# Kernel tuning notes

Measured on AMD Instinct MI355X. Metric: run time of the kernel, lower is better.

The kernel has to match this reference:

```python
import jax, jax.numpy as jnp
import numpy as np

SCORE_THRESH = 0.05
IOU_THRESH = 0.5
TOP_K = 1000      # candidates fed to NMS
MAX_DET = 100     # padded output detections


def _build_anchors(H, W):
    """Standard RetinaNet anchors: levels P3..P7, 3 ratios x 3 scales."""
    ratios = np.array([0.5, 1.0, 2.0])
    scales = np.array([2 ** 0, 2 ** (1.0 / 3.0), 2 ** (2.0 / 3.0)])
    all_anchors = []
    for lvl in [3, 4, 5, 6, 7]:
        stride = 2 ** lvl
        base_size = 2 ** (lvl + 2)
        # 9 base anchors centered at origin (ratio-major, scale-minor ordering)
        s = base_size * np.tile(scales, len(ratios))          # [9]
        r = np.repeat(ratios, len(scales))                    # [9]
        areas = s * s
        w = np.sqrt(areas / r)
        h = w * r
        base = np.stack([-w / 2, -h / 2, w / 2, h / 2], axis=1)  # [9,4]
        fh = (H + stride - 1) // stride
        fw = (W + stride - 1) // stride
        sx = (np.arange(fw) + 0.5) * stride
        sy = (np.arange(fh) + 0.5) * stride
        gx, gy = np.meshgrid(sx, sy)
        shifts = np.stack([gx.ravel(), gy.ravel(), gx.ravel(), gy.ravel()], axis=1)  # [fh*fw,4]
        all_anchors.append((shifts[:, None, :] + base[None, :, :]).reshape(-1, 4))
    return np.concatenate(all_anchors, axis=0).astype(np.float32)  # [A,4]


def setup_inputs() -> dict:
    key = jax.random.key(0)
    k1, k2 = jax.random.split(key)
    H = W = 1024
    C = 80
    anchors = jnp.asarray(_build_anchors(H, W))[None]            # [1,A,4]
    A = anchors.shape[1]
    classifications = jax.random.uniform(k1, (1, A, C), dtype=jnp.float32)
    regressions = jax.random.normal(k2, (1, A, 4), dtype=jnp.float32)
    return {"classifications": classifications, "regressions": regressions,
            "anchors": anchors, "img_h": H, "img_w": W}


def _decode_clip(anchors, regressions, img_h, img_w):
    # BBoxTransform with mean 0, std [0.1,0.1,0.2,0.2]
    aw = anchors[..., 2] - anchors[..., 0]
    ah = anchors[..., 3] - anchors[..., 1]
    acx = anchors[..., 0] + 0.5 * aw
    acy = anchors[..., 1] + 0.5 * ah
    dx = regressions[..., 0] * 0.1
    dy = regressions[..., 1] * 0.1
    dw = regressions[..., 2] * 0.2
    dh = regressions[..., 3] * 0.2
    pcx = acx + dx * aw
    pcy = acy + dy * ah
    pw = jnp.exp(dw) * aw
    ph = jnp.exp(dh) * ah
    boxes = jnp.stack([pcx - 0.5 * pw, pcy - 0.5 * ph,
                       pcx + 0.5 * pw, pcy + 0.5 * ph], axis=-1)
    # ClipBoxes
    lo = jnp.zeros(4, boxes.dtype)
    hi = jnp.array([img_w, img_h, img_w, img_h], boxes.dtype)
    return jnp.clip(boxes, lo, hi)  # [1,A,4]


def _nms_keep(boxes, valid):
    """Sequential greedy NMS over score-sorted boxes [K,4]; returns keep mask [K]."""
    K = boxes.shape[0]
    areas = jnp.maximum(boxes[:, 2] - boxes[:, 0], 0) * jnp.maximum(boxes[:, 3] - boxes[:, 1], 0)
    idx = jnp.arange(K)

    def body(i, keep):
        b = boxes[i]
        xx1 = jnp.maximum(b[0], boxes[:, 0])
        yy1 = jnp.maximum(b[1], boxes[:, 1])
        xx2 = jnp.minimum(b[2], boxes[:, 2])
        yy2 = jnp.minimum(b[3], boxes[:, 3])
        inter = jnp.maximum(xx2 - xx1, 0) * jnp.maximum(yy2 - yy1, 0)
        iou = inter / (areas[i] + areas - inter + 1e-8)
        suppress = (iou > IOU_THRESH) & (idx > i)
        return jnp.where(keep[i], keep & ~suppress, keep)

    return jax.lax.fori_loop(0, K, body, valid)


def reference(classifications, regressions, anchors, img_h, img_w):
    boxes = _decode_clip(anchors, regressions, img_h, img_w)       # [1,A,4]
    scores = jnp.max(classifications, axis=2)                      # [1,A]
    # Score threshold: mask out low scores, keep fixed shape (padded NMS)
    s0 = jnp.where(scores[0] > SCORE_THRESH, scores[0], -1.0)      # [A]
    top_scores, top_idx = jax.lax.top_k(s0, TOP_K)                 # sorted desc
    cand_boxes = boxes[0, top_idx]                                 # [K,4]
    keep = _nms_keep(cand_boxes, top_scores > SCORE_THRESH)        # [K]
    final = jnp.where(keep, top_scores, -1.0)
    det_scores, sel = jax.lax.top_k(final, MAX_DET)                # [100]
    det_idx = top_idx[sel]                                         # indices into A
    det_valid = det_scores > SCORE_THRESH
    cls = classifications[0, det_idx]                              # [100,C]
    nms_scores = jnp.where(det_valid, jnp.max(cls, axis=1), 0.0)
    nms_class = jnp.where(det_valid, jnp.argmax(cls, axis=1), -1)
    det_boxes = jnp.where(det_valid[:, None], boxes[0, det_idx], 0.0)
    return (nms_scores, nms_class, det_boxes)
```

## Files before the change

kernel.cpp:

```cpp
#include <hip/hip_runtime.h>
#include <stdint.h>

#define SCORE_THRESH 0.05f
#define IOU_THRESH 0.5f
#define TOP_K 1000
#define MAX_DET 100

#define D0_BITS 13
#define D0_BINS 8192
#define D1_BITS 12
#define D1_BINS 4096
#define NREP 4
#define CAND_CAP 2048
#define NMS_CHUNK 128

typedef unsigned int u32;
typedef unsigned long long u64;

#define OFF_HIST0    0
#define OFF_HIST1    131072
#define OFF_STATE    196608
#define OFF_BAR      197632
#define MEMSET_LEN   218112
#define OFF_CAND     218112
#define OFF_RFLAG    226304
#define OFF_SIDX     230304
#define OFF_SSCORE   234304
#define OFF_CBOX     238304
#define OFF_M        254304
#define OFF_SCORES   382304

#define BAR_STRIDE_U32 1024

__device__ __forceinline__ u32 order_f32(float f) {
    u32 b = __float_as_uint(f);
    return (b & 0x80000000u) ? ~b : (b | 0x80000000u);
}

__device__ __forceinline__ void st_sc(u32* p, u32 v)   { __hip_atomic_store(p, v, __ATOMIC_RELAXED, __HIP_MEMORY_SCOPE_AGENT); }
__device__ __forceinline__ void st_sc(float* p, float v){ __hip_atomic_store(p, v, __ATOMIC_RELAXED, __HIP_MEMORY_SCOPE_AGENT); }
__device__ __forceinline__ void st_sc(u64* p, u64 v)   { __hip_atomic_store(p, v, __ATOMIC_RELAXED, __HIP_MEMORY_SCOPE_AGENT); }
__device__ __forceinline__ u32  ld_sc(u32* p)          { return __hip_atomic_load(p, __ATOMIC_RELAXED, __HIP_MEMORY_SCOPE_AGENT); }

__device__ __forceinline__ void gbar(u32* barr, int k, int b, u32 gsz, bool dowait) {
    __syncthreads();
    if (threadIdx.x == 0) {
        asm volatile("s_waitcnt vmcnt(0)" ::: "memory");
        u32* base = barr + (size_t)k * BAR_STRIDE_U32;
        int g = b & 7;
        if (__hip_atomic_fetch_add(base + g * 32, 1u, __ATOMIC_RELAXED,
                                   __HIP_MEMORY_SCOPE_AGENT) == gsz - 1u)
            __hip_atomic_fetch_add(base + 8 * 32, 1u, __ATOMIC_RELAXED,
                                   __HIP_MEMORY_SCOPE_AGENT);
        if (dowait) {
            while (ld_sc(base + 8 * 32) < 8u)
                __builtin_amdgcn_s_sleep(8);
        }
        asm volatile("" ::: "memory");
    }
    __syncthreads();
}

union ShMem {
    u32 hl[D0_BINS / 2];
    u32 wtot[4];
    struct { u32 wcnt[4]; u32 wbase[4]; u32 bbase; } cmp;
    struct { u64 ckeys[8]; u32 wpart[4][8]; } rank;
    struct {
        u64 Ml[2 * NMS_CHUNK * 16];
        u64 keepS[16];
        u32 nib[256];
        int act[TOP_K];
        u32 wsum[4];
        int nactS;
        int det[MAX_DET];
    } nms;
};

__global__ void __launch_bounds__(256, 2)
mega(const float* __restrict__ cls, const float* __restrict__ regs,
     const float* __restrict__ anchors, const int* __restrict__ pH,
     const int* __restrict__ pW, int A, int C,
     char* __restrict__ ws, float* __restrict__ out)
{
    __shared__ ShMem sh;
    __shared__ u32 shcut[3];
    u32*   hist0  = (u32*)(ws + OFF_HIST0);
    u32*   hist1  = (u32*)(ws + OFF_HIST1);
    u32*   state  = (u32*)(ws + OFF_STATE);
    u32*   barr   = (u32*)(ws + OFF_BAR);
    u32*   cand   = (u32*)(ws + OFF_CAND);
    u32*   rflag  = (u32*)(ws + OFF_RFLAG);
    u32*   sidx   = (u32*)(ws + OFF_SIDX);
    float* sscore = (float*)(ws + OFF_SSCORE);
    float* cbox   = (float*)(ws + OFF_CBOX);
    u64*   M      = (u64*)(ws + OFF_M);
    float* scores = (float*)(ws + OFF_SCORES);

    const int t = threadIdx.x;
    const int b = blockIdx.x;
    const int G = gridDim.x;
    const int gid = b * 256 + t;
    const int gstride = G * 256;
    const int lane = t & 63, wv = t >> 6;
    const u32 gsz = (u32)(G >> 3);

    if (C == 80) {
        for (int i = t; i < D0_BINS / 2; i += 256) sh.hl[i] = 0;
        __syncthreads();
        int sub = t & 3;
        int la  = t >> 2;
        int nstrips = (A + 63) >> 6;
        int per = (nstrips + G - 1) / G;
        for (int s = 0; s < per; s++) {
            int a = (b * per + s) * 64 + la;
            float m = -1e30f;
            if (a < A) {
                const float* p = cls + (size_t)a * 80 + sub * 4;
                #pragma unroll
                for (int k2 = 0; k2 < 5; k2++) {
                    float4 v = *(const float4*)(p + k2 * 16);
                    m = fmaxf(m, fmaxf(fmaxf(v.x, v.y), fmaxf(v.z, v.w)));
                }
            }
            m = fmaxf(m, __shfl_xor(m, 1, 64));
            m = fmaxf(m, __shfl_xor(m, 2, 64));
            if (sub == 0 && a < A) {
                float s0 = (m > SCORE_THRESH) ? m : -1.0f;
                st_sc(&scores[a], s0);
                u32 d = order_f32(s0) >> (32 - D0_BITS);
                atomicAdd(&sh.hl[d >> 1], (d & 1) ? 0x10000u : 1u);
            }
        }
        __syncthreads();
        u32* rep = hist0 + (size_t)(b & (NREP - 1)) * D0_BINS;
        for (int i = t; i < D0_BINS / 2; i += 256) {
            u32 v = sh.hl[i];
            if (v & 0xFFFFu) atomicAdd(&rep[2 * i],     v & 0xFFFFu);
            if (v >> 16)     atomicAdd(&rep[2 * i + 1], v >> 16);
        }
    } else {
        u32* rep = hist0 + (size_t)(b & (NREP - 1)) * D0_BINS;
        for (int a = gid; a < A; a += gstride) {
            const float* p = cls + (size_t)a * C;
            float m = -1e30f;
            for (int c = 0; c < C; c++) m = fmaxf(m, p[c]);
            float s0 = (m > SCORE_THRESH) ? m : -1.0f;
            st_sc(&scores[a], s0);
            atomicAdd(&rep[order_f32(s0) >> (32 - D0_BITS)], 1u);
        }
    }
    gbar(barr, 0, b, gsz, true);

    {
        u32 cnt[32];
        #pragma unroll
        for (int i = 0; i < 32; i++) cnt[i] = 0;
        const uint4* hp = (const uint4*)hist0;
        #pragma unroll
        for (int r = 0; r < NREP; r++) {
            #pragma unroll
            for (int i = 0; i < 8; i++) {
                uint4 v = hp[r * (D0_BINS / 4) + t * 8 + i];
                cnt[4*i]   += v.x; cnt[4*i+1] += v.y;
                cnt[4*i+2] += v.z; cnt[4*i+3] += v.w;
            }
        }
        u32 s = 0;
        #pragma unroll
        for (int i = 0; i < 32; i++) s += cnt[i];
        u32 x = s;
        for (int off = 1; off < 64; off <<= 1) {
            u32 v = (u32)__shfl_down((int)x, off, 64);
            if (lane + off < 64) x += v;
        }
        if (lane == 0) sh.wtot[wv] = x;
        __syncthreads();
        u32 above = x - s;
        for (int w = wv + 1; w < 4; w++) above += sh.wtot[w];
        if (above < TOP_K && above + s >= TOP_K) {
            u32 cum = above;
            for (int i = 31; i >= 0; i--) {
                cum += cnt[i];
                if (cum >= TOP_K) {
                    shcut[0] = (u32)(t * 32 + i);
                    shcut[1] = TOP_K - (cum - cnt[i]);
                    break;
                }
            }
        }
        __syncthreads();
    }
    const u32 d0cut = shcut[0];
    const u32 krem  = shcut[1];

    {
        u32* rep1 = hist1 + (size_t)(b & (NREP - 1)) * D1_BINS;
        for (int a = gid; a < A; a += gstride) {
            u32 key = order_f32(scores[a]);
            if ((key >> (32 - D0_BITS)) == d0cut)
                atomicAdd(&rep1[(key >> 7) & (D1_BINS - 1)], 1u);
        }
    }
    gbar(barr, 1, b, gsz, true);

    {
        u32 cnt[16];
        #pragma unroll
        for (int i = 0; i < 16; i++) cnt[i] = 0;
        const uint4* hp = (const uint4*)hist1;
        #pragma unroll
        for (int r = 0; r < NREP; r++) {
            #pragma unroll
            for (int i = 0; i < 4; i++) {
                uint4 v = hp[r * (D1_BINS / 4) + t * 4 + i];
                cnt[4*i]   += v.x; cnt[4*i+1] += v.y;
                cnt[4*i+2] += v.z; cnt[4*i+3] += v.w;
            }
        }
        u32 s = 0;
        #pragma unroll
        for (int i = 0; i < 16; i++) s += cnt[i];
        u32 x = s;
        for (int off = 1; off < 64; off <<= 1) {
            u32 v = (u32)__shfl_down((int)x, off, 64);
            if (lane + off < 64) x += v;
        }
        if (lane == 0) sh.wtot[wv] = x;
        __syncthreads();
        u32 above = x - s;
        for (int w = wv + 1; w < 4; w++) above += sh.wtot[w];
        if (above < krem && above + s >= krem) {
            u32 cum = above;
            for (int i = 15; i >= 0; i--) {
                cum += cnt[i];
                if (cum >= krem) { shcut[2] = (u32)(t * 16 + i); break; }
            }
        }
        __syncthreads();
    }
    const u32 cut25 = (d0cut << D1_BITS) | shcut[2];

    {
        int nr = (A + gstride - 1) / gstride;
        u32 mycnt = 0;
        for (int r = 0; r < nr; r++) {
            int a = gid + r * gstride;
            mycnt += ((a < A) && ((order_f32(scores[a]) >> 7) >= cut25)) ? 1u : 0u;
        }
        u32 wc = mycnt;
        wc += (u32)__shfl_xor((int)wc, 1, 64);
        wc += (u32)__shfl_xor((int)wc, 2, 64);
        wc += (u32)__shfl_xor((int)wc, 4, 64);
        wc += (u32)__shfl_xor((int)wc, 8, 64);
        wc += (u32)__shfl_xor((int)wc, 16, 64);
        wc += (u32)__shfl_xor((int)wc, 32, 64);
        if (lane == 0) sh.cmp.wcnt[wv] = wc;
        __syncthreads();
        if (t == 0) {
            u32 s = 0;
            #pragma unroll
            for (int w = 0; w < 4; w++) { sh.cmp.wbase[w] = s; s += sh.cmp.wcnt[w]; }
            sh.cmp.bbase = s ? atomicAdd(&state[5 * 32], s) : 0u;
        }
        __syncthreads();
        u32 off = sh.cmp.bbase + sh.cmp.wbase[wv];
        for (int r = 0; r < nr; r++) {
            int a = gid + r * gstride;
            bool pass = (a < A) && ((order_f32(scores[a]) >> 7) >= cut25);
            u64 mask = __ballot(pass ? 1 : 0);
            if (pass) {
                u32 pos = off + (u32)__popcll(mask & ((1ull << lane) - 1ull));
                if (pos < CAND_CAP) st_sc(&cand[pos], (u32)a);
            }
            off += (u32)__popcll(mask);
        }
    }
    gbar(barr, 2, b, gsz, b < CAND_CAP / 8);

    if (b < CAND_CAP / 8) {
        int n = (int)state[5 * 32]; if (n > CAND_CAP) n = CAND_CAP;
        u64 kj[8];
        #pragma unroll
        for (int q = 0; q < 8; q++) {
            int j = t * 8 + q;
            u64 kk = 0ull;
            if (j < n) {
                u32 a = cand[j];
                kk = ((u64)order_f32(scores[a]) << 32) | (u64)(0xFFFFFFFFu - a);
            }
            kj[q] = kk;
        }
        for (int bb = b; bb < CAND_CAP / 8; bb += G) {
            if (t < 8) {
                int c = bb * 8 + t;
                u64 ck = 0ull;
                if (c < n) {
                    u32 a = cand[c];
                    ck = ((u64)order_f32(scores[a]) << 32) | (u64)(0xFFFFFFFFu - a);
                }
                sh.rank.ckeys[t] = ck;
            }
            __syncthreads();
            u64 ck[8];
            #pragma unroll
            for (int q = 0; q < 8; q++) ck[q] = sh.rank.ckeys[q];
            u32 cnt8[8] = {0,0,0,0,0,0,0,0};
            #pragma unroll
            for (int q = 0; q < 8; q++) {
                u64 kq = kj[q];
                #pragma unroll
                for (int q2 = 0; q2 < 8; q2++) cnt8[q2] += (kq > ck[q2]) ? 1u : 0u;
            }
            #pragma unroll
            for (int q2 = 0; q2 < 8; q2++) {
                u32 x = cnt8[q2];
                x += (u32)__shfl_xor((int)x, 1, 64);
                x += (u32)__shfl_xor((int)x, 2, 64);
                x += (u32)__shfl_xor((int)x, 4, 64);
                x += (u32)__shfl_xor((int)x, 8, 64);
                x += (u32)__shfl_xor((int)x, 16, 64);
                x += (u32)__shfl_xor((int)x, 32, 64);
                if (lane == 0) sh.rank.wpart[wv][q2] = x;
            }
            __syncthreads();
            if (t < 8) {
                int c = bb * 8 + t;
                if (c < n) {
                    u32 rank = sh.rank.wpart[0][t] + sh.rank.wpart[1][t]
                             + sh.rank.wpart[2][t] + sh.rank.wpart[3][t];
                    if (rank < TOP_K) {
                        u32 a = cand[c];
                        st_sc(&sidx[rank], a);
                        st_sc(&sscore[rank], scores[a]);
                        float4 an = *(const float4*)(anchors + (size_t)a * 4);
                        float4 rg = *(const float4*)(regs + (size_t)a * 4);
                        float aw = an.z - an.x, ah = an.w - an.y;
                        float acx = an.x + 0.5f * aw, acy = an.y + 0.5f * ah;
                        float pcx = acx + (rg.x * 0.1f) * aw;
                        float pcy = acy + (rg.y * 0.1f) * ah;
                        float pw = expf(rg.z * 0.2f) * aw;
                        float ph = expf(rg.w * 0.2f) * ah;
                        float W = (float)(*pW), H = (float)(*pH);
                        st_sc(&cbox[rank * 4 + 0], fminf(fmaxf(pcx - 0.5f * pw, 0.0f), W));
                        st_sc(&cbox[rank * 4 + 1], fminf(fmaxf(pcy - 0.5f * ph, 0.0f), H));
                        st_sc(&cbox[rank * 4 + 2], fminf(fmaxf(pcx + 0.5f * pw, 0.0f), W));
                        st_sc(&cbox[rank * 4 + 3], fminf(fmaxf(pcy + 0.5f * ph, 0.0f), H));
                    }
                }
            }
            __syncthreads();
        }
    }
    gbar(barr, 3, b, gsz, b * 4 < TOP_K);

    {
        const float4* B4 = (const float4*)cbox;
        for (int i = b * 4 + wv; i < TOP_K; i += G * 4) {
            float4 bi = B4[i];
            float ai = fmaxf(bi.z - bi.x, 0.0f) * fmaxf(bi.w - bi.y, 0.0f);
            u64 any = 0ull;
            for (int w = 0; w < 16; w++) {
                int j = w * 64 + lane;
                bool sup = false;
                if (j < TOP_K && j > i) {
                    float4 bj = B4[j];
                    float aj = fmaxf(bj.z - bj.x, 0.0f) * fmaxf(bj.w - bj.y, 0.0f);
                    float xx1 = fmaxf(bi.x, bj.x), yy1 = fmaxf(bi.y, bj.y);
                    float xx2 = fminf(bi.z, bj.z), yy2 = fminf(bi.w, bj.w);
                    float inter = fmaxf(xx2 - xx1, 0.0f) * fmaxf(yy2 - yy1, 0.0f);
                    float iou = inter / (ai + aj - inter + 1e-8f);
                    sup = iou > IOU_THRESH;
                }
                u64 mask = __ballot(sup ? 1 : 0);
                if (lane == 0) { st_sc(&M[(size_t)i * 16 + w], mask); any |= mask; }
            }
            if (lane == 0) st_sc(&rflag[i], (any != 0ull) ? 1u : 0u);
        }
    }
    gbar(barr, 4, b, gsz, b == 0);

    if (b == 0) {
        {
            u32 nb = 0;
            int j0 = 4 * t;
            #pragma unroll
            for (int q = 0; q < 4; q++) {
                int j = j0 + q;
                if (j < TOP_K && sscore[j] > SCORE_THRESH) nb |= (1u << q);
            }
            sh.nms.nib[t] = nb;
        }
        u32 flags = 0; int cnt = 0;
        {
            int r0 = 4 * t;
            #pragma unroll
            for (int q = 0; q < 4; q++) {
                int r = r0 + q;
                if (r < TOP_K && rflag[r]) { flags |= (1u << q); cnt++; }
            }
        }
        int x = cnt;
        for (int off = 1; off < 64; off <<= 1) {
            int v = __shfl_up(x, off, 64);
            if (lane >= off) x += v;
        }
        if (lane == 63) sh.nms.wsum[wv] = (u32)x;
        __syncthreads();
        if (t < 16) {
            u64 w = 0;
            for (int m2 = 0; m2 < 16; m2++)
                w |= ((u64)sh.nms.nib[t * 16 + m2]) << (4 * m2);
            sh.nms.keepS[t] = w;
        }
        int base = 0;
        for (int w = 0; w < wv; w++) base += (int)sh.nms.wsum[w];
        int pos = base + x - cnt;
        {
            int r0 = 4 * t;
            #pragma unroll
            for (int q = 0; q < 4; q++)
                if (flags & (1u << q)) sh.nms.act[pos++] = r0 + q;
        }
        if (t == 0) {
            int na = 0;
            for (int w = 0; w < 4; w++) na += (int)sh.nms.wsum[w];
            sh.nms.nactS = na;
        }
        __syncthreads();
        int nact = sh.nms.nactS;
        int nchunks = (nact + NMS_CHUNK - 1) / NMS_CHUNK;

        if (nchunks > 0) {
            int cn0 = (nact < NMS_CHUNK) ? nact : NMS_CHUNK;
            for (int i = t; i < cn0 * 16; i += 256) {
                int row = sh.nms.act[i >> 4];
                sh.nms.Ml[i] = M[(size_t)row * 16 + (i & 15)];
            }
        }
        __syncthreads();
        u64 kp = (wv == 0 && lane < 16) ? sh.nms.keepS[lane] : 0ull;
        for (int ci = 0; ci < nchunks; ci++) {
            int c0 = ci * NMS_CHUNK;
            int cn = (nact - c0 < NMS_CHUNK) ? (nact - c0) : NMS_CHUNK;
            int cur = (ci & 1) * (NMS_CHUNK * 16);
            if (ci + 1 < nchunks && t >= 64) {
                int c0n = c0 + NMS_CHUNK;
                int cnn = (nact - c0n < NMS_CHUNK) ? (nact - c0n) : NMS_CHUNK;
                int nxt = ((ci + 1) & 1) * (NMS_CHUNK * 16);
                for (int i = t - 64; i < cnn * 16; i += 192) {
                    int row = sh.nms.act[c0n + (i >> 4)];
                    sh.nms.Ml[nxt + i] = M[(size_t)row * 16 + (i & 15)];
                }
            }
            if (wv == 0) {
                u64 mreg = (lane < 16 && cn > 0) ? sh.nms.Ml[cur + lane] : 0ull;
                for (int k = 0; k < cn; k++) {
                    u64 mnx = (lane < 16 && k + 1 < cn)
                            ? sh.nms.Ml[cur + (k + 1) * 16 + lane] : 0ull;
                    int i = sh.nms.act[c0 + k];
                    u64 kw = __shfl(kp, i >> 6, 64);
                    if ((kw >> (i & 63)) & 1ull) kp &= ~mreg;
                    mreg = mnx;
                }
            }
            __syncthreads();
        }
        if (wv == 0 && lane < 16) sh.nms.keepS[lane] = kp;
        __syncthreads();

        if (t == 0) {
            int cnt2 = 0;
            for (int w = 0; w < 16 && cnt2 < MAX_DET; w++) {
                u64 kw = sh.nms.keepS[w];
                while (kw && cnt2 < MAX_DET) {
                    int bbit = __ffsll((unsigned long long)kw) - 1;
                    sh.nms.det[cnt2++] = w * 64 + bbit;
                    kw &= kw - 1;
                }
            }
            for (; cnt2 < MAX_DET; cnt2++) sh.nms.det[cnt2] = -1;
        }
        __syncthreads();
        if (t < MAX_DET) {
            int i = sh.nms.det[t];
            if (i >= 0) {
                u32 a = sidx[i];
                const float* p = cls + (size_t)a * C;
                float best = -1e30f; int bc = 0;
                if (C == 80) {
                    #pragma unroll
                    for (int c4 = 0; c4 < 20; c4++) {
                        float4 v = *(const float4*)(p + c4 * 4);
                        if (v.x > best) { best = v.x; bc = c4 * 4; }
                        if (v.y > best) { best = v.y; bc = c4 * 4 + 1; }
                        if (v.z > best) { best = v.z; bc = c4 * 4 + 2; }
                        if (v.w > best) { best = v.w; bc = c4 * 4 + 3; }
                    }
                } else {
                    best = p[0]; bc = 0;
                    for (int c = 1; c < C; c++) {
                        float v = p[c];
                        if (v > best) { best = v; bc = c; }
                    }
                }
                out[t] = best;
                out[MAX_DET + t] = (float)bc;
                out[2 * MAX_DET + t * 4 + 0] = cbox[i * 4 + 0];
                out[2 * MAX_DET + t * 4 + 1] = cbox[i * 4 + 1];
                out[2 * MAX_DET + t * 4 + 2] = cbox[i * 4 + 2];
                out[2 * MAX_DET + t * 4 + 3] = cbox[i * 4 + 3];
            } else {
                out[t] = 0.0f;
                out[MAX_DET + t] = -1.0f;
                out[2 * MAX_DET + t * 4 + 0] = 0.0f;
                out[2 * MAX_DET + t * 4 + 1] = 0.0f;
                out[2 * MAX_DET + t * 4 + 2] = 0.0f;
                out[2 * MAX_DET + t * 4 + 3] = 0.0f;
            }
        }
    }
}

extern "C" void kernel_launch(void* const* d_in, const int* in_sizes, int n_in,
                              void* d_out, int out_size, void* d_ws, size_t ws_size,
                              hipStream_t stream) {
    (void)n_in; (void)out_size; (void)ws_size;
    const float* cls     = (const float*)d_in[0];
    const float* regs    = (const float*)d_in[1];
    const float* anchors = (const float*)d_in[2];
    const int*   pH      = (const int*)d_in[3];
    const int*   pW      = (const int*)d_in[4];
    int A = in_sizes[1] / 4;
    int C = in_sizes[0] / A;

    static int nCU = 0;
    if (nCU <= 0) {
        int dev = 0;
        hipGetDevice(&dev);
        hipDeviceGetAttribute(&nCU, hipDeviceAttributeMultiprocessorCount, dev);
        if (nCU <= 0) nCU = 256;
    }
    int G = (2 * nCU) & ~7;
    if (G < 8) G = 8;

    char* ws = (char*)d_ws;
    hipMemsetAsync(ws, 0, MEMSET_LEN, stream);
    mega<<<dim3(G), dim3(256), 0, stream>>>(cls, regs, anchors, pH, pW, A, C,
                                            ws, (float*)d_out);
}
```

Baseline: 169.3 us.

## Replace two-pass radix top-k select with single histogram on 1-score, flag-array barrier

Bins scores by the float bits of (1 - score) into 4096 bins, which gives fine resolution near score 1, so a single histogram pass finds the top-k cutoff bin. This removes the second histogram pass over all anchors and one grid barrier. The grid barrier becomes per-block flags that block 0 polls and then releases the others with a single flag. The coarser cut can admit more candidates into the rank stage, bounded by CAND_CAP, and the number of blocks is now capped at 512.

```diff
diff --git a/kernel.cpp b/kernel.cpp
--- a/kernel.cpp
+++ b/kernel.cpp
@@ -6,10 +6,7 @@
 #define TOP_K 1000
 #define MAX_DET 100
 
-#define D0_BITS 13
-#define D0_BINS 8192
-#define D1_BITS 12
-#define D1_BINS 4096
+#define UBINS 4096
 #define NREP 4
 #define CAND_CAP 2048
 #define NMS_CHUNK 128
@@ -17,18 +14,17 @@
 typedef unsigned int u32;
 typedef unsigned long long u64;
 
-#define OFF_HIST0    0
-#define OFF_HIST1    131072
-#define OFF_STATE    196608
-#define OFF_BAR      197632
-#define MEMSET_LEN   218112
-#define OFF_CAND     218112
-#define OFF_RFLAG    226304
-#define OFF_SIDX     230304
-#define OFF_SSCORE   234304
-#define OFF_CBOX     238304
-#define OFF_M        254304
-#define OFF_SCORES   382304
+#define OFF_HIST     0
+#define OFF_STATE    65536
+#define OFF_BAR      66560
+#define MEMSET_LEN   82944
+#define OFF_CAND     82944
+#define OFF_RFLAG    91136
+#define OFF_SIDX     95136
+#define OFF_SSCORE   99136
+#define OFF_CBOX     103136
+#define OFF_M        119136
+#define OFF_SCORES   247136
 
 #define BAR_STRIDE_U32 1024
 
@@ -37,32 +33,43 @@
     return (b & 0x80000000u) ? ~b : (b | 0x80000000u);
 }
 
+__device__ __forceinline__ u32 ubin(float s0) {
+    float u = 1.0f - s0;
+    u32 bin = __float_as_uint(u) >> 18;
+    return bin > (UBINS - 1) ? (UBINS - 1) : bin;
+}
+
 __device__ __forceinline__ void st_sc(u32* p, u32 v)   { __hip_atomic_store(p, v, __ATOMIC_RELAXED, __HIP_MEMORY_SCOPE_AGENT); }
 __device__ __forceinline__ void st_sc(float* p, float v){ __hip_atomic_store(p, v, __ATOMIC_RELAXED, __HIP_MEMORY_SCOPE_AGENT); }
 __device__ __forceinline__ void st_sc(u64* p, u64 v)   { __hip_atomic_store(p, v, __ATOMIC_RELAXED, __HIP_MEMORY_SCOPE_AGENT); }
 __device__ __forceinline__ u32  ld_sc(u32* p)          { return __hip_atomic_load(p, __ATOMIC_RELAXED, __HIP_MEMORY_SCOPE_AGENT); }
 
-__device__ __forceinline__ void gbar(u32* barr, int k, int b, u32 gsz, bool dowait) {
+__device__ __forceinline__ void gbar(u32* barr, int k, int b, int G, bool dowait) {
     __syncthreads();
+    u32* base = barr + (size_t)k * BAR_STRIDE_U32;
     if (threadIdx.x == 0) {
         asm volatile("s_waitcnt vmcnt(0)" ::: "memory");
-        u32* base = barr + (size_t)k * BAR_STRIDE_U32;
-        int g = b & 7;
-        if (__hip_atomic_fetch_add(base + g * 32, 1u, __ATOMIC_RELAXED,
-                                   __HIP_MEMORY_SCOPE_AGENT) == gsz - 1u)
-            __hip_atomic_fetch_add(base + 8 * 32, 1u, __ATOMIC_RELAXED,
-                                   __HIP_MEMORY_SCOPE_AGENT);
-        if (dowait) {
-            while (ld_sc(base + 8 * 32) < 8u)
-                __builtin_amdgcn_s_sleep(8);
-        }
-        asm volatile("" ::: "memory");
+        st_sc(&base[b], 1u);
+    }
+    if (!dowait) return;
+    if (b == 0) {
+        for (;;) {
+            int my = 1;
+            for (int i = (int)threadIdx.x; i < G; i += 256) my &= (int)ld_sc(&base[i]);
+            if (__syncthreads_and(my)) break;
+        }
+        if (threadIdx.x == 0) st_sc(&base[512], 1u);
+    } else {
+        if (threadIdx.x == 0) {
+            while (ld_sc(&base[512]) == 0u) __builtin_amdgcn_s_sleep(8);
+        }
     }
     __syncthreads();
+    asm volatile("" ::: "memory");
 }
 
 union ShMem {
-    u32 hl[D0_BINS / 2];
+    u32 hl[UBINS / 2];
     u32 wtot[4];
     struct { u32 wcnt[4]; u32 wbase[4]; u32 bbase; } cmp;
     struct { u64 ckeys[8]; u32 wpart[4][8]; } rank;
@@ -84,9 +91,8 @@
      char* __restrict__ ws, float* __restrict__ out)
 {
     __shared__ ShMem sh;
-    __shared__ u32 shcut[3];
-    u32*   hist0  = (u32*)(ws + OFF_HIST0);
-    u32*   hist1  = (u32*)(ws + OFF_HIST1);
+    __shared__ u32 shcut;
+    u32*   hist   = (u32*)(ws + OFF_HIST);
     u32*   state  = (u32*)(ws + OFF_STATE);
     u32*   barr   = (u32*)(ws + OFF_BAR);
     u32*   cand   = (u32*)(ws + OFF_CAND);
@@ -103,10 +109,9 @@
     const int gid = b * 256 + t;
     const int gstride = G * 256;
     const int lane = t & 63, wv = t >> 6;
-    const u32 gsz = (u32)(G >> 3);
 
     if (C == 80) {
-        for (int i = t; i < D0_BINS / 2; i += 256) sh.hl[i] = 0;
+        for (int i = t; i < UBINS / 2; i += 256) sh.hl[i] = 0;
         __syncthreads();
         int sub = t & 3;
         int la  = t >> 2;
@@ -128,92 +133,41 @@
             if (sub == 0 && a < A) {
                 float s0 = (m > SCORE_THRESH) ? m : -1.0f;
                 st_sc(&scores[a], s0);
-                u32 d = order_f32(s0) >> (32 - D0_BITS);
+                u32 d = ubin(s0);
                 atomicAdd(&sh.hl[d >> 1], (d & 1) ? 0x10000u : 1u);
             }
         }
         __syncthreads();
-        u32* rep = hist0 + (size_t)(b & (NREP - 1)) * D0_BINS;
-        for (int i = t; i < D0_BINS / 2; i += 256) {
+        u32* rep = hist + (size_t)(b & (NREP - 1)) * UBINS;
+        for (int i = t; i < UBINS / 2; i += 256) {
             u32 v = sh.hl[i];
             if (v & 0xFFFFu) atomicAdd(&rep[2 * i],     v & 0xFFFFu);
             if (v >> 16)     atomicAdd(&rep[2 * i + 1], v >> 16);
         }
     } else {
-        u32* rep = hist0 + (size_t)(b & (NREP - 1)) * D0_BINS;
+        u32* rep = hist + (size_t)(b & (NREP - 1)) * UBINS;
         for (int a = gid; a < A; a += gstride) {
             const float* p = cls + (size_t)a * C;
             float m = -1e30f;
             for (int c = 0; c < C; c++) m = fmaxf(m, p[c]);
             float s0 = (m > SCORE_THRESH) ? m : -1.0f;
             st_sc(&scores[a], s0);
-            atomicAdd(&rep[order_f32(s0) >> (32 - D0_BITS)], 1u);
-        }
-    }
-    gbar(barr, 0, b, gsz, true);
+            atomicAdd(&rep[ubin(s0)], 1u);
+        }
+    }
+    gbar(barr, 0, b, G, true);
 
     {
-        u32 cnt[32];
-        #pragma unroll
-        for (int i = 0; i < 32; i++) cnt[i] = 0;
-        const uint4* hp = (const uint4*)hist0;
-        #pragma unroll
-        for (int r = 0; r < NREP; r++) {
-            #pragma unroll
-            for (int i = 0; i < 8; i++) {
-                uint4 v = hp[r * (D0_BINS / 4) + t * 8 + i];
-                cnt[4*i]   += v.x; cnt[4*i+1] += v.y;
-                cnt[4*i+2] += v.z; cnt[4*i+3] += v.w;
-            }
-        }
-        u32 s = 0;
-        #pragma unroll
-        for (int i = 0; i < 32; i++) s += cnt[i];
-        u32 x = s;
-        for (int off = 1; off < 64; off <<= 1) {
-            u32 v = (u32)__shfl_down((int)x, off, 64);
-            if (lane + off < 64) x += v;
-        }
-        if (lane == 0) sh.wtot[wv] = x;
-        __syncthreads();
-        u32 above = x - s;
-        for (int w = wv + 1; w < 4; w++) above += sh.wtot[w];
-        if (above < TOP_K && above + s >= TOP_K) {
-            u32 cum = above;
-            for (int i = 31; i >= 0; i--) {
-                cum += cnt[i];
-                if (cum >= TOP_K) {
-                    shcut[0] = (u32)(t * 32 + i);
-                    shcut[1] = TOP_K - (cum - cnt[i]);
-                    break;
-                }
-            }
-        }
-        __syncthreads();
-    }
-    const u32 d0cut = shcut[0];
-    const u32 krem  = shcut[1];
-
-    {
-        u32* rep1 = hist1 + (size_t)(b & (NREP - 1)) * D1_BINS;
-        for (int a = gid; a < A; a += gstride) {
-            u32 key = order_f32(scores[a]);
-            if ((key >> (32 - D0_BITS)) == d0cut)
-                atomicAdd(&rep1[(key >> 7) & (D1_BINS - 1)], 1u);
-        }
-    }
-    gbar(barr, 1, b, gsz, true);
-
-    {
+        if (t == 0) shcut = UBINS - 1;
         u32 cnt[16];
         #pragma unroll
         for (int i = 0; i < 16; i++) cnt[i] = 0;
-        const uint4* hp = (const uint4*)hist1;
+        const uint4* hp = (const uint4*)hist;
         #pragma unroll
         for (int r = 0; r < NREP; r++) {
             #pragma unroll
             for (int i = 0; i < 4; i++) {
-                uint4 v = hp[r * (D1_BINS / 4) + t * 4 + i];
+                uint4 v = hp[r * (UBINS / 4) + t * 4 + i];
                 cnt[4*i]   += v.x; cnt[4*i+1] += v.y;
                 cnt[4*i+2] += v.z; cnt[4*i+3] += v.w;
             }
@@ -223,30 +177,30 @@
         for (int i = 0; i < 16; i++) s += cnt[i];
         u32 x = s;
         for (int off = 1; off < 64; off <<= 1) {
-            u32 v = (u32)__shfl_down((int)x, off, 64);
-            if (lane + off < 64) x += v;
-        }
-        if (lane == 0) sh.wtot[wv] = x;
-        __syncthreads();
-        u32 above = x - s;
-        for (int w = wv + 1; w < 4; w++) above += sh.wtot[w];
-        if (above < krem && above + s >= krem) {
-            u32 cum = above;
-            for (int i = 15; i >= 0; i--) {
+            u32 v = (u32)__shfl_up((int)x, off, 64);
+            if (lane >= off) x += v;
+        }
+        if (lane == 63) sh.wtot[wv] = x;
+        __syncthreads();
+        u32 below = x - s;
+        for (int w = 0; w < wv; w++) below += sh.wtot[w];
+        if (below < TOP_K && below + s >= TOP_K) {
+            u32 cum = below;
+            for (int i = 0; i < 16; i++) {
                 cum += cnt[i];
-                if (cum >= krem) { shcut[2] = (u32)(t * 16 + i); break; }
-            }
-        }
-        __syncthreads();
-    }
-    const u32 cut25 = (d0cut << D1_BITS) | shcut[2];
+                if (cum >= TOP_K) { shcut = (u32)(t * 16 + i); break; }
+            }
+        }
+        __syncthreads();
+    }
+    const u32 cutbin = shcut;
 
     {
         int nr = (A + gstride - 1) / gstride;
         u32 mycnt = 0;
         for (int r = 0; r < nr; r++) {
             int a = gid + r * gstride;
-            mycnt += ((a < A) && ((order_f32(scores[a]) >> 7) >= cut25)) ? 1u : 0u;
+            mycnt += ((a < A) && (ubin(scores[a]) <= cutbin)) ? 1u : 0u;
         }
         u32 wc = mycnt;
         wc += (u32)__shfl_xor((int)wc, 1, 64);
@@ -267,7 +221,7 @@
         u32 off = sh.cmp.bbase + sh.cmp.wbase[wv];
         for (int r = 0; r < nr; r++) {
             int a = gid + r * gstride;
-            bool pass = (a < A) && ((order_f32(scores[a]) >> 7) >= cut25);
+            bool pass = (a < A) && (ubin(scores[a]) <= cutbin);
             u64 mask = __ballot(pass ? 1 : 0);
             if (pass) {
                 u32 pos = off + (u32)__popcll(mask & ((1ull << lane) - 1ull));
@@ -276,7 +230,7 @@
             off += (u32)__popcll(mask);
         }
     }
-    gbar(barr, 2, b, gsz, b < CAND_CAP / 8);
+    gbar(barr, 1, b, G, b < CAND_CAP / 8);
 
     if (b < CAND_CAP / 8) {
         int n = (int)state[5 * 32]; if (n > CAND_CAP) n = CAND_CAP;
@@ -352,7 +306,7 @@
             __syncthreads();
         }
     }
-    gbar(barr, 3, b, gsz, b * 4 < TOP_K);
+    gbar(barr, 2, b, G, b * 4 < TOP_K);
 
     {
         const float4* B4 = (const float4*)cbox;
@@ -378,7 +332,7 @@
             if (lane == 0) st_sc(&rflag[i], (any != 0ull) ? 1u : 0u);
         }
     }
-    gbar(barr, 4, b, gsz, b == 0);
+    gbar(barr, 3, b, G, b == 0);
 
     if (b == 0) {
         {
@@ -541,7 +495,8 @@
         hipDeviceGetAttribute(&nCU, hipDeviceAttributeMultiprocessorCount, dev);
         if (nCU <= 0) nCU = 256;
     }
-    int G = (2 * nCU) & ~7;
+    int G = 2 * nCU;
+    if (G > 512) G = 512;
     if (G < 8) G = 8;
 
     char* ws = (char*)d_ws;
```

Result: faster. 153.3 us (-9.4%).
